# Performance work log

Measured on AMD Instinct MI355X. Metric: run time of the kernel, lower is better.

## Reference

```python
import jax, jax.numpy as jnp
import numpy as np

B, L, HID, NH = 2, 2048, 1024, 16
HD = HID // NH  # 64


def setup_inputs() -> dict:
    key = jax.random.key(0)
    ks = jax.random.split(key, 12)
    s = 1.0 / np.sqrt(HID)
    query = jax.random.normal(ks[0], (B, L, HID), jnp.float32)
    key_t = jax.random.normal(ks[1], (B, L, HID), jnp.float32)
    value = jax.random.normal(ks[2], (B, L, HID), jnp.float32)
    # key padding mask: True = valid token; random lengths in [1024, 2048]
    lengths = jax.random.randint(ks[3], (B,), L // 2, L + 1)
    key_mask = jnp.arange(L)[None, :] < lengths[:, None]  # [B, K] bool
    # attn_mask: True = blocked (causal upper triangle), 2D branch [Q, K]
    attn_mask = jnp.triu(jnp.ones((L, L), jnp.bool_), k=1)
    Wq = jax.random.normal(ks[4], (HID, HID), jnp.float32) * s
    Wk = jax.random.normal(ks[5], (HID, HID), jnp.float32) * s
    Wv = jax.random.normal(ks[6], (HID, HID), jnp.float32) * s
    Wo = jax.random.normal(ks[7], (HID, HID), jnp.float32) * s
    bq = jax.random.normal(ks[8], (HID,), jnp.float32) * 0.01
    bk = jax.random.normal(ks[9], (HID,), jnp.float32) * 0.01
    bv = jax.random.normal(ks[10], (HID,), jnp.float32) * 0.01
    bo = jax.random.normal(ks[11], (HID,), jnp.float32) * 0.01
    return {"query": query, "key": key_t, "value": value,
            "key_mask": key_mask, "attn_mask": attn_mask,
            "Wq": Wq, "bq": bq, "Wk": Wk, "bk": bk,
            "Wv": Wv, "bv": bv, "Wo": Wo, "bo": bo}


def reference(query, key, value, key_mask, attn_mask,
              Wq, bq, Wk, bk, Wv, bv, Wo, bo):
    Bq, Q, _ = query.shape
    K = key.shape[1]
    # projections (torch Linear: x @ W.T + b), split heads -> [B, H, L, HD]
    def proj(x, W, b, L_):
        return (x @ W.T + b).reshape(Bq, L_, NH, HD).transpose(0, 2, 1, 3)
    q = proj(query, Wq, bq, Q)
    k = proj(key, Wk, bk, K)
    v = proj(value, Wv, bv, K)
    scores = jnp.einsum('bhqd,bhkd->bhqk', q, k) / np.sqrt(HD)
    blocked = attn_mask[None, None, :, :]                 # True = blocked
    kmask = key_mask[:, None, None, :]                    # True = valid
    valid = (~blocked) & kmask                            # [B,H,Q,K] (bcast)
    scores = jnp.where(blocked, -10000.0, scores)
    scores = jnp.where(kmask, scores, -10000.0)
    weights = jax.nn.softmax(scores, axis=-1)
    weights = weights * valid.astype(weights.dtype)
    weights = weights / jnp.maximum(weights.sum(-1, keepdims=True), 1e-6)
    attended = jnp.einsum('bhqk,bhkd->bhqd', weights, v)
    attended = attended.transpose(0, 2, 1, 3).reshape(Bq, Q, HID)
    return attended @ Wo.T + bo
```

## Files before the change

kernel.cpp:

```cpp
#include <hip/hip_runtime.h>
#include <hip/hip_bf16.h>
#include <stdint.h>


#define L_SEQ 2048
#define HID 1024
#define NHEAD 16
#define HD 64

typedef __attribute__((ext_vector_type(8))) short bf16x8;
typedef __attribute__((ext_vector_type(8))) unsigned short u16x8;
typedef __attribute__((ext_vector_type(4))) float f32x4;

__device__ __forceinline__ unsigned short f2bf(float f) {
  unsigned int u = __builtin_bit_cast(unsigned int, f);
  u += 0x7fffu + ((u >> 16) & 1u);
  return (unsigned short)(u >> 16);
}

__device__ __forceinline__ unsigned int pk2bf(float a, float b) {
  unsigned int r;
  asm("v_cvt_pk_bf16_f32 %0, %1, %2" : "=v"(r) : "v"(a), "v"(b));
  return r;
}

__device__ __forceinline__ void gl_lds16(const void* g, void* l) {
  __builtin_amdgcn_global_load_lds(
      (const __attribute__((address_space(1))) unsigned int*)(uintptr_t)g,
      (__attribute__((address_space(3))) unsigned int*)(uint32_t)(uintptr_t)l,
      16, 0, 0);
}

__device__ __forceinline__ f32x4 mfma16(bf16x8 a, bf16x8 b, f32x4 c) {
  return __builtin_amdgcn_mfma_f32_16x16x32_bf16(a, b, c, 0, 0, 0);
}

__global__ __launch_bounds__(256)
void convert_all_kernel(const float* __restrict__ q, const float* __restrict__ k,
                        const float* __restrict__ v, const float* __restrict__ wq,
                        const float* __restrict__ wk, const float* __restrict__ wv,
                        const float* __restrict__ wo, const unsigned int* __restrict__ km,
                        unsigned short* __restrict__ qb, unsigned short* __restrict__ kb,
                        unsigned short* __restrict__ vb, unsigned short* __restrict__ wqb,
                        unsigned short* __restrict__ wkb, unsigned short* __restrict__ wvb,
                        unsigned short* __restrict__ wob, int* __restrict__ lens) {
  __shared__ int red[256];
  const int bid = blockIdx.x;
  const int t = threadIdx.x;
  if (bid == 8192) {
    unsigned int w0 = km[0];
    bool u8mode = (w0 != 1u);
    for (int b = 0; b < 2; ++b) {
      int cnt = 0;
      if (u8mode) {
        const unsigned char* p = (const unsigned char*)km + b * L_SEQ;
        for (int i = t; i < L_SEQ; i += 256) cnt += (p[i] != 0) ? 1 : 0;
      } else {
        const unsigned int* p = km + b * L_SEQ;
        for (int i = t; i < L_SEQ; i += 256) cnt += (p[i] != 0) ? 1 : 0;
      }
      red[t] = cnt;
      __syncthreads();
      for (int s = 128; s > 0; s >>= 1) {
        if (t < s) red[t] += red[t + s];
        __syncthreads();
      }
      if (t == 0) lens[b] = red[0];
      __syncthreads();
    }
    return;
  }
  const float* src;
  unsigned short* dst;
  int base;
  if (bid < 6144) {
    int s = bid >> 11;
    base = (bid & 2047) * 2048;
    src = s == 0 ? q : (s == 1 ? k : v);
    dst = s == 0 ? qb : (s == 1 ? kb : vb);
  } else {
    int r = bid - 6144;
    int s = r >> 9;
    base = (r & 511) * 2048;
    src = s == 0 ? wq : (s == 1 ? wk : (s == 2 ? wv : wo));
    dst = s == 0 ? wqb : (s == 1 ? wkb : (s == 2 ? wvb : wob));
  }
  int i = base + t * 8;
  float4 a = *(const float4*)(src + i);
  float4 b4 = *(const float4*)(src + i + 4);
  u16x8 o;
  o[0] = f2bf(a.x); o[1] = f2bf(a.y); o[2] = f2bf(a.z); o[3] = f2bf(a.w);
  o[4] = f2bf(b4.x); o[5] = f2bf(b4.y); o[6] = f2bf(b4.z); o[7] = f2bf(b4.w);
  *(u16x8*)(dst + i) = o;
}

__device__ __forceinline__ void gemm128_bf_core(const unsigned short* __restrict__ A,
                                                const unsigned short* __restrict__ W,
                                                int m0, int n0, int K,
                                                unsigned short* As, unsigned short* Bs,
                                                f32x4 acc[4][4]) {
  const int tid = threadIdx.x;
  const int w = tid >> 6, lane = tid & 63;
  const int l15 = lane & 15, l4 = lane >> 4;
  const int wr = w >> 1, wc = w & 1;
#pragma unroll
  for (int i = 0; i < 4; ++i)
#pragma unroll
    for (int j = 0; j < 4; ++j) acc[i][j] = (f32x4){0.f, 0.f, 0.f, 0.f};

  const int nk = K >> 5;
#pragma unroll
  for (int i = 0; i < 2; ++i) {
    int c = i * 256 + tid;
    int row = c >> 2, col = (c & 3) * 8;
    gl_lds16(A + (size_t)(m0 + row) * K + col, (char*)As + (i * 256 + w * 64) * 16);
    gl_lds16(W + (size_t)(n0 + row) * K + col, (char*)Bs + (i * 256 + w * 64) * 16);
  }
  __syncthreads();

  int cur = 0;
  for (int t = 0; t < nk; ++t) {
    const int k0 = t * 32;
    if (t + 1 < nk) {
#pragma unroll
      for (int i = 0; i < 2; ++i) {
        int c = i * 256 + tid;
        int row = c >> 2, col = (c & 3) * 8;
        gl_lds16(A + (size_t)(m0 + row) * K + k0 + 32 + col,
                 (char*)As + (cur ^ 1) * 8192 + (i * 256 + w * 64) * 16);
        gl_lds16(W + (size_t)(n0 + row) * K + k0 + 32 + col,
                 (char*)Bs + (cur ^ 1) * 8192 + (i * 256 + w * 64) * 16);
      }
    }
    const unsigned short* Asb = As + cur * 4096;
    const unsigned short* Bsb = Bs + cur * 4096;
    bf16x8 af[4], bfr[4];
#pragma unroll
    for (int i = 0; i < 4; ++i)
      af[i] = *(const bf16x8*)(Asb + (wr * 64 + i * 16 + l15) * 32 + l4 * 8);
#pragma unroll
    for (int j = 0; j < 4; ++j)
      bfr[j] = *(const bf16x8*)(Bsb + (wc * 64 + j * 16 + l15) * 32 + l4 * 8);
    __builtin_amdgcn_s_setprio(1);
#pragma unroll
    for (int i = 0; i < 4; ++i)
#pragma unroll
      for (int j = 0; j < 4; ++j) acc[i][j] = mfma16(af[i], bfr[j], acc[i][j]);
    __builtin_amdgcn_s_setprio(0);
    __syncthreads();
    cur ^= 1;
  }
}

__global__ __launch_bounds__(256)
void qkv_gemm_kernel(const unsigned short* __restrict__ qb, const unsigned short* __restrict__ kb,
                     const unsigned short* __restrict__ vb, const unsigned short* __restrict__ wq,
                     const unsigned short* __restrict__ wk, const unsigned short* __restrict__ wv,
                     const float* __restrict__ bq, const float* __restrict__ bk,
                     const float* __restrict__ bv, unsigned short* __restrict__ Qp,
                     unsigned short* __restrict__ Kp, unsigned short* __restrict__ Vtp) {
  __shared__ unsigned short As[2 * 128 * 32];
  __shared__ unsigned short Bs[2 * 128 * 32];
  const int id = blockIdx.x;
  const int g = (id & 7) * 96 + (id >> 3);
  const int mg = g >> 3;
  const int z = mg >> 5;
  const int m0 = (mg & 31) * 128;
  const int n0 = (g & 7) * 128;

  const unsigned short* A = z == 0 ? qb : (z == 1 ? kb : vb);
  const unsigned short* W = z == 0 ? wq : (z == 1 ? wk : wv);
  const float* bias = z == 0 ? bq : (z == 1 ? bk : bv);
  f32x4 acc[4][4];
  gemm128_bf_core(A, W, m0, n0, HID, As, Bs, acc);

  const int tid = threadIdx.x;
  const int w = tid >> 6, lane = tid & 63;
  const int l15 = lane & 15, l4 = lane >> 4;
  const int wr = w >> 1, wc = w & 1;
  const float scale = (z == 0) ? 0.125f * 1.44269504089f : 1.0f;
  if (z == 2) {
#pragma unroll
    for (int i = 0; i < 4; ++i)
#pragma unroll
      for (int j = 0; j < 4; ++j) {
        int grow0 = m0 + wr * 64 + i * 16 + l4 * 4;
        int gcol = n0 + wc * 64 + j * 16 + l15;
        float bv_ = bias[gcol];
        int bb = grow0 >> 11, ll0 = grow0 & 2047;
        int hh = gcol >> 6, d = gcol & 63;
        uint2 pw;
        pw.x = pk2bf(acc[i][j][0] + bv_, acc[i][j][1] + bv_);
        pw.y = pk2bf(acc[i][j][2] + bv_, acc[i][j][3] + bv_);
        *(uint2*)(&Vtp[((size_t)(bb * NHEAD + hh) * HD + d) * L_SEQ + ll0]) = pw;
      }
  } else {
    unsigned short* P = (z == 0) ? Qp : Kp;
#pragma unroll
    for (int i = 0; i < 4; ++i)
#pragma unroll
      for (int j = 0; j < 4; ++j)
#pragma unroll
        for (int r = 0; r < 4; ++r) {
          int grow = m0 + wr * 64 + i * 16 + l4 * 4 + r;
          int gcol = n0 + wc * 64 + j * 16 + l15;
          float v = (acc[i][j][r] + bias[gcol]) * scale;
          int bb = grow >> 11, ll = grow & 2047;
          int hh = gcol >> 6, d = gcol & 63;
          P[((size_t)(bb * NHEAD + hh) * L_SEQ + ll) * HD + d] = f2bf(v);
        }
  }
}

__global__ __launch_bounds__(256)
void out_gemm_kernel(const unsigned short* __restrict__ att, const unsigned short* __restrict__ wo,
                     const float* __restrict__ bo, float* __restrict__ out) {
  __shared__ unsigned short As[2 * 128 * 32];
  __shared__ unsigned short Bs[2 * 128 * 32];
  const int id = blockIdx.x;
  const int swz = (id & 7) * 32 + (id >> 3);
  const int m0 = (swz >> 3) * 128, n0 = (swz & 7) * 128;
  f32x4 acc[4][4];
  gemm128_bf_core(att, wo, m0, n0, HID, As, Bs, acc);

  const int tid = threadIdx.x;
  const int w = tid >> 6, lane = tid & 63;
  const int l15 = lane & 15, l4 = lane >> 4;
  const int wr = w >> 1, wc = w & 1;
#pragma unroll
  for (int i = 0; i < 4; ++i)
#pragma unroll
    for (int j = 0; j < 4; ++j)
#pragma unroll
      for (int r = 0; r < 4; ++r) {
        int grow = m0 + wr * 64 + i * 16 + l4 * 4 + r;
        int gcol = n0 + wc * 64 + j * 16 + l15;
        out[(size_t)grow * HID + gcol] = acc[i][j][r] + bo[gcol];
      }
}

__global__ __launch_bounds__(512)
void attn_kernel(const unsigned short* __restrict__ Qp, const unsigned short* __restrict__ Kp,
                 const unsigned short* __restrict__ Vtp, unsigned short* __restrict__ att,
                 const int* __restrict__ lens) {
  __shared__ unsigned short Ks[2][64 * 64];
  __shared__ unsigned short Vs[2][64 * 64];
  __shared__ unsigned short Ps[8][16 * 72];

  const int id = blockIdx.x;
  const int g = (id & 7) * 64 + (id >> 3);
  const int bh = g >> 4;
  const int x = g & 15;
  const int b = bh >> 4, h = bh & 15;
  const int tid = threadIdx.x, w = tid >> 6, lane = tid & 63;
  const int l15 = lane & 15, l4 = lane >> 4;
  const int len = lens[b];
  const int sub = (w < 4) ? x : (31 - x);
  const int qw0 = sub * 64 + (w & 3) * 16;

  const unsigned short* Qg = Qp + (size_t)bh * L_SEQ * HD;
  const unsigned short* Kg = Kp + (size_t)bh * L_SEQ * HD;
  const unsigned short* Vg = Vtp + (size_t)bh * HD * L_SEQ;

  const int rr = tid >> 3, cb = tid & 7;
  const int swz = (cb ^ (rr & 7)) * 8;
  const unsigned short* KgRow = Kg + (size_t)rr * HD + swz;
  const unsigned short* VgRow = Vg + (size_t)rr * L_SEQ + swz;

  bf16x8 qf[2];
#pragma unroll
  for (int kk = 0; kk < 2; ++kk)
    qf[kk] = *(const bf16x8*)(Qg + (size_t)(qw0 + l15) * HD + kk * 32 + l4 * 8);

  f32x4 acc[4];
#pragma unroll
  for (int n = 0; n < 4; ++n) acc[n] = (f32x4){0.f, 0.f, 0.f, 0.f};
  float mq = -1e30f, lq = 0.f;

  int koff[4][2];
#pragma unroll
  for (int n = 0; n < 4; ++n)
#pragma unroll
    for (int kk = 0; kk < 2; ++kk) {
      int row = n * 16 + l15;
      koff[n][kk] = row * 128 + (((l4 + kk * 4) ^ (row & 7)) * 16);
    }

  const int len_r = ((len + 63) >> 6) << 6;
  const int hi_end = 64 * (32 - x);
  const int kv_end = (hi_end < len_r) ? hi_end : len_r;
  const int nt = kv_end >> 6;

  gl_lds16(KgRow, (char*)&Ks[0][0] + w * 1024);
  gl_lds16(VgRow, (char*)&Vs[0][0] + w * 1024);
  __syncthreads();

  int cur = 0;
  for (int t = 0; t < nt; ++t) {
    const int k0 = t * 64;
    if (t + 1 < nt) {
      const int k1 = k0 + 64;
      gl_lds16(KgRow + (size_t)k1 * HD, (char*)&Ks[cur ^ 1][0] + w * 1024);
      gl_lds16(VgRow + k1, (char*)&Vs[cur ^ 1][0] + w * 1024);
    }
    if (k0 <= qw0 + 15) {
      const char* Kb = (const char*)&Ks[cur][0];
      const char* Vb = (const char*)&Vs[cur][0];
      f32x4 s[4];
#pragma unroll
      for (int n = 0; n < 4; ++n) s[n] = (f32x4){0.f, 0.f, 0.f, 0.f};
      __builtin_amdgcn_s_setprio(1);
#pragma unroll
      for (int kk = 0; kk < 2; ++kk) {
#pragma unroll
        for (int n = 0; n < 4; ++n)
          s[n] = mfma16(*(const bf16x8*)(Kb + koff[n][kk]), qf[kk], s[n]);
      }
      __builtin_amdgcn_s_setprio(0);
      if (!(k0 + 63 <= qw0 && k0 + 64 <= len)) {
        const int qa = qw0 + l15;
#pragma unroll
        for (int n = 0; n < 4; ++n)
#pragma unroll
          for (int r = 0; r < 4; ++r) {
            int ka = k0 + n * 16 + l4 * 4 + r;
            if (ka > qa || ka >= len) s[n][r] = -1e30f;
          }
      }
      float v01 = fmaxf(fmaxf(s[0][0], s[0][1]), fmaxf(s[0][2], s[0][3]));
      float v23 = fmaxf(fmaxf(s[1][0], s[1][1]), fmaxf(s[1][2], s[1][3]));
      float v45 = fmaxf(fmaxf(s[2][0], s[2][1]), fmaxf(s[2][2], s[2][3]));
      float v67 = fmaxf(fmaxf(s[3][0], s[3][1]), fmaxf(s[3][2], s[3][3]));
      float v = fmaxf(fmaxf(v01, v23), fmaxf(v45, v67));
      v = fmaxf(v, __shfl_xor(v, 16));
      v = fmaxf(v, __shfl_xor(v, 32));
      if (!__all(v - mq <= 8.0f)) {
        float mnew = fmaxf(mq, v);
        float alpha = __builtin_amdgcn_exp2f(mq - mnew);
        mq = mnew;
        float ar[4];
#pragma unroll
        for (int r = 0; r < 4; ++r) ar[r] = __shfl(alpha, l4 * 4 + r, 64);
#pragma unroll
        for (int n = 0; n < 4; ++n)
#pragma unroll
          for (int r = 0; r < 4; ++r) acc[n][r] *= ar[r];
        lq *= alpha;
      }
      float rs = 0.f;
#pragma unroll
      for (int n = 0; n < 4; ++n)
#pragma unroll
        for (int r = 0; r < 4; ++r) {
          float p = __builtin_amdgcn_exp2f(s[n][r] - mq);
          s[n][r] = p;
          rs += p;
        }
      rs += __shfl_xor(rs, 16);
      rs += __shfl_xor(rs, 32);
      lq += rs;
#pragma unroll
      for (int n = 0; n < 4; ++n) {
        uint2 pw;
        pw.x = pk2bf(s[n][0], s[n][1]);
        pw.y = pk2bf(s[n][2], s[n][3]);
        *(uint2*)(&Ps[w][l15 * 72 + n * 16 + l4 * 4]) = pw;
      }
      bf16x8 pf[2];
#pragma unroll
      for (int kk = 0; kk < 2; ++kk)
        pf[kk] = *(const bf16x8*)(&Ps[w][l15 * 72 + kk * 32 + l4 * 8]);
      __builtin_amdgcn_s_setprio(1);
#pragma unroll
      for (int kk = 0; kk < 2; ++kk) {
#pragma unroll
        for (int n = 0; n < 4; ++n)
          acc[n] = mfma16(pf[kk], *(const bf16x8*)(Vb + koff[n][kk]), acc[n]);
      }
      __builtin_amdgcn_s_setprio(0);
    }
    __syncthreads();
    cur ^= 1;
  }

  float invq = 1.0f / lq;
  float invr[4];
#pragma unroll
  for (int r = 0; r < 4; ++r) invr[r] = __shfl(invq, l4 * 4 + r, 64);
#pragma unroll
  for (int r = 0; r < 4; ++r) {
    int qa = qw0 + l4 * 4 + r;
#pragma unroll
    for (int n = 0; n < 4; ++n)
      att[((size_t)(b * L_SEQ + qa)) * HID + h * HD + n * 16 + l15] = f2bf(acc[n][r] * invr[r]);
  }
}

extern "C" void kernel_launch(void* const* d_in, const int* in_sizes, int n_in,
                              void* d_out, int out_size, void* d_ws, size_t ws_size,
                              hipStream_t stream) {
  const float* query = (const float*)d_in[0];
  const float* key = (const float*)d_in[1];
  const float* value = (const float*)d_in[2];
  const unsigned int* key_mask = (const unsigned int*)d_in[3];
  const float* Wq = (const float*)d_in[5];
  const float* bq = (const float*)d_in[6];
  const float* Wk = (const float*)d_in[7];
  const float* bk = (const float*)d_in[8];
  const float* Wv = (const float*)d_in[9];
  const float* bv = (const float*)d_in[10];
  const float* Wo = (const float*)d_in[11];
  const float* bo = (const float*)d_in[12];

  char* ws = (char*)d_ws;
  const size_t SZ_X = (size_t)4096 * 1024 * 2;
  const size_t SZ_W = (size_t)1024 * 1024 * 2;
  unsigned short* qb = (unsigned short*)(ws);
  unsigned short* kb = (unsigned short*)(ws + SZ_X);
  unsigned short* vb = (unsigned short*)(ws + 2 * SZ_X);
  unsigned short* wqb = (unsigned short*)(ws + 3 * SZ_X);
  unsigned short* wkb = (unsigned short*)(ws + 3 * SZ_X + SZ_W);
  unsigned short* wvb = (unsigned short*)(ws + 3 * SZ_X + 2 * SZ_W);
  unsigned short* wob = (unsigned short*)(ws + 3 * SZ_X + 3 * SZ_W);
  unsigned short* Qp = (unsigned short*)(ws + 3 * SZ_X + 4 * SZ_W);
  unsigned short* Kp = (unsigned short*)(ws + 4 * SZ_X + 4 * SZ_W);
  unsigned short* Vtp = (unsigned short*)(ws + 5 * SZ_X + 4 * SZ_W);
  unsigned short* att = (unsigned short*)(ws + 6 * SZ_X + 4 * SZ_W);
  int* lens = (int*)(ws + 7 * SZ_X + 4 * SZ_W);

  convert_all_kernel<<<8193, 256, 0, stream>>>(query, key, value, Wq, Wk, Wv, Wo, key_mask,
                                               qb, kb, vb, wqb, wkb, wvb, wob, lens);
  qkv_gemm_kernel<<<768, 256, 0, stream>>>(qb, kb, vb, wqb, wkb, wvb, bq, bk, bv,
                                           Qp, Kp, Vtp);
  attn_kernel<<<512, 512, 0, stream>>>(Qp, Kp, Vtp, att, lens);
  out_gemm_kernel<<<256, 256, 0, stream>>>(att, wob, bo, (float*)d_out);
}
```

Before: 125.5 us.

## Triple-buffer GEMM LDS pipeline with explicit vmcnt waits and single barrier

Replaces the double-buffered GEMM mainloop, used by the QKV and output projections, with a three-stage LDS ring. Loads run two K-tiles ahead, and the loop waits with explicit s_waitcnt vmcnt counts plus a raw s_barrier instead of __syncthreads. The goal is to hide more global-load latency behind MFMA work and cut stalls at the barrier. In exchange, LDS per block grows by half, which may lower occupancy, and correctness now depends on the hand-set vmcnt counts.

```diff
diff --git a/kernel.cpp b/kernel.cpp
--- a/kernel.cpp
+++ b/kernel.cpp
@@ -94,11 +94,11 @@
   *(u16x8*)(dst + i) = o;
 }
 
-__device__ __forceinline__ void gemm128_bf_core(const unsigned short* __restrict__ A,
-                                                const unsigned short* __restrict__ W,
-                                                int m0, int n0, int K,
-                                                unsigned short* As, unsigned short* Bs,
-                                                f32x4 acc[4][4]) {
+__device__ __forceinline__ void gemm128_pipe3_core(const unsigned short* __restrict__ A,
+                                                   const unsigned short* __restrict__ W,
+                                                   int m0, int n0, int K,
+                                                   unsigned short* As, unsigned short* Bs,
+                                                   f32x4 acc[4][4]) {
   const int tid = threadIdx.x;
   const int w = tid >> 6, lane = tid & 63;
   const int l15 = lane & 15, l4 = lane >> 4;
@@ -109,31 +109,43 @@
     for (int j = 0; j < 4; ++j) acc[i][j] = (f32x4){0.f, 0.f, 0.f, 0.f};
 
   const int nk = K >> 5;
-#pragma unroll
-  for (int i = 0; i < 2; ++i) {
-    int c = i * 256 + tid;
-    int row = c >> 2, col = (c & 3) * 8;
-    gl_lds16(A + (size_t)(m0 + row) * K + col, (char*)As + (i * 256 + w * 64) * 16);
-    gl_lds16(W + (size_t)(n0 + row) * K + col, (char*)Bs + (i * 256 + w * 64) * 16);
-  }
-  __syncthreads();
-
-  int cur = 0;
+  const int c0 = tid, c1 = 256 + tid;
+  const int r0 = c0 >> 2, o0 = (c0 & 3) * 8;
+  const int r1 = c1 >> 2, o1 = (c1 & 3) * 8;
+  const unsigned short* A0 = A + (size_t)(m0 + r0) * K + o0;
+  const unsigned short* A1 = A + (size_t)(m0 + r1) * K + o1;
+  const unsigned short* W0 = W + (size_t)(n0 + r0) * K + o0;
+  const unsigned short* W1 = W + (size_t)(n0 + r1) * K + o1;
+  const int base0 = (w * 64) * 16;
+  const int base1 = (256 + w * 64) * 16;
+
+  gl_lds16(A0, (char*)As + base0);
+  gl_lds16(W0, (char*)Bs + base0);
+  gl_lds16(A1, (char*)As + base1);
+  gl_lds16(W1, (char*)Bs + base1);
+  gl_lds16(A0 + 32, (char*)As + 8192 + base0);
+  gl_lds16(W0 + 32, (char*)Bs + 8192 + base0);
+  gl_lds16(A1 + 32, (char*)As + 8192 + base1);
+  gl_lds16(W1 + 32, (char*)Bs + 8192 + base1);
+  asm volatile("s_waitcnt vmcnt(4)" ::: "memory");
+  __builtin_amdgcn_s_barrier();
+  asm volatile("" ::: "memory");
+
+  int bc = 0;
   for (int t = 0; t < nk; ++t) {
-    const int k0 = t * 32;
-    if (t + 1 < nk) {
-#pragma unroll
-      for (int i = 0; i < 2; ++i) {
-        int c = i * 256 + tid;
-        int row = c >> 2, col = (c & 3) * 8;
-        gl_lds16(A + (size_t)(m0 + row) * K + k0 + 32 + col,
-                 (char*)As + (cur ^ 1) * 8192 + (i * 256 + w * 64) * 16);
-        gl_lds16(W + (size_t)(n0 + row) * K + k0 + 32 + col,
-                 (char*)Bs + (cur ^ 1) * 8192 + (i * 256 + w * 64) * 16);
-      }
-    }
-    const unsigned short* Asb = As + cur * 4096;
-    const unsigned short* Bsb = Bs + cur * 4096;
+    if (t + 2 < nk) {
+      int bs = bc + 2;
+      if (bs >= 3) bs -= 3;
+      const int kk = (t + 2) * 32;
+      char* a = (char*)As + bs * 8192;
+      char* b = (char*)Bs + bs * 8192;
+      gl_lds16(A0 + kk, a + base0);
+      gl_lds16(W0 + kk, b + base0);
+      gl_lds16(A1 + kk, a + base1);
+      gl_lds16(W1 + kk, b + base1);
+    }
+    const unsigned short* Asb = As + bc * 4096;
+    const unsigned short* Bsb = Bs + bc * 4096;
     bf16x8 af[4], bfr[4];
 #pragma unroll
     for (int i = 0; i < 4; ++i)
@@ -147,8 +159,16 @@
 #pragma unroll
       for (int j = 0; j < 4; ++j) acc[i][j] = mfma16(af[i], bfr[j], acc[i][j]);
     __builtin_amdgcn_s_setprio(0);
-    __syncthreads();
-    cur ^= 1;
+    if (t + 1 < nk) {
+      if (t + 2 < nk)
+        asm volatile("s_waitcnt vmcnt(4)" ::: "memory");
+      else
+        asm volatile("s_waitcnt vmcnt(0)" ::: "memory");
+      __builtin_amdgcn_s_barrier();
+      asm volatile("" ::: "memory");
+      ++bc;
+      if (bc == 3) bc = 0;
+    }
   }
 }
 
@@ -159,8 +179,8 @@
                      const float* __restrict__ bq, const float* __restrict__ bk,
                      const float* __restrict__ bv, unsigned short* __restrict__ Qp,
                      unsigned short* __restrict__ Kp, unsigned short* __restrict__ Vtp) {
-  __shared__ unsigned short As[2 * 128 * 32];
-  __shared__ unsigned short Bs[2 * 128 * 32];
+  __shared__ unsigned short As[3 * 128 * 32];
+  __shared__ unsigned short Bs[3 * 128 * 32];
   const int id = blockIdx.x;
   const int g = (id & 7) * 96 + (id >> 3);
   const int mg = g >> 3;
@@ -172,7 +192,7 @@
   const unsigned short* W = z == 0 ? wq : (z == 1 ? wk : wv);
   const float* bias = z == 0 ? bq : (z == 1 ? bk : bv);
   f32x4 acc[4][4];
-  gemm128_bf_core(A, W, m0, n0, HID, As, Bs, acc);
+  gemm128_pipe3_core(A, W, m0, n0, HID, As, Bs, acc);
 
   const int tid = threadIdx.x;
   const int w = tid >> 6, lane = tid & 63;
@@ -215,13 +235,13 @@
 __global__ __launch_bounds__(256)
 void out_gemm_kernel(const unsigned short* __restrict__ att, const unsigned short* __restrict__ wo,
                      const float* __restrict__ bo, float* __restrict__ out) {
-  __shared__ unsigned short As[2 * 128 * 32];
-  __shared__ unsigned short Bs[2 * 128 * 32];
+  __shared__ unsigned short As[3 * 128 * 32];
+  __shared__ unsigned short Bs[3 * 128 * 32];
   const int id = blockIdx.x;
   const int swz = (id & 7) * 32 + (id >> 3);
   const int m0 = (swz >> 3) * 128, n0 = (swz & 7) * 128;
   f32x4 acc[4][4];
-  gemm128_bf_core(att, wo, m0, n0, HID, As, Bs, acc);
+  gemm128_pipe3_core(att, wo, m0, n0, HID, As, Bs, acc);
 
   const int tid = threadIdx.x;
   const int w = tid >> 6, lane = tid & 63;
```

Result: faster. 120.9 us (-3.6%).
